# Performance work log

Hardware: AMD Instinct MI355X
Metric: run time of the kernel (lower is better)

## Reference

```python
import jax, jax.numpy as jnp
import numpy as np
import math

B, L, E, H, G = 2, 128, 1024, 16, 8
D = E // H   # head_dim = 64
R = H // G   # query heads per kv head = 2


def setup_inputs() -> dict:
    key = jax.random.key(0)
    ks = jax.random.split(key, 12)
    def nrm(k, shape, s=1.0):
        return jax.random.normal(k, shape, dtype=jnp.float32) * s
    return {
        "Q": nrm(ks[0], (B, L, E)),
        "K": nrm(ks[1], (B, L, E)),
        "V": nrm(ks[2], (B, L, E)),
        "rpe": nrm(ks[3], (B, L, L, E)),
        "ln_g": jnp.ones((E,), jnp.float32),
        "ln_b": jnp.zeros((E,), jnp.float32),
        "Wq": nrm(ks[4], (E, H * D), 0.02), "bq": jnp.zeros((H * D,), jnp.float32),
        "Wk": nrm(ks[5], (E, G * D), 0.02), "bk": jnp.zeros((G * D,), jnp.float32),
        "Wv": nrm(ks[6], (E, G * D), 0.02), "bv": jnp.zeros((G * D,), jnp.float32),
        "Wrk": nrm(ks[7], (E, G * D), 0.02), "brk": jnp.zeros((G * D,), jnp.float32),
        "Wrv": nrm(ks[8], (E, G * D), 0.02), "brv": jnp.zeros((G * D,), jnp.float32),
        "Wo": nrm(ks[9], (E, E), 0.02), "bo": jnp.zeros((E,), jnp.float32),
    }


def _layernorm(x, g, b, eps=1e-5):
    mu = jnp.mean(x, axis=-1, keepdims=True)
    var = jnp.var(x, axis=-1, keepdims=True)
    return (x - mu) * jax.lax.rsqrt(var + eps) * g + b


def reference(Q, K, V, rpe, ln_g, ln_b, Wq, bq, Wk, bk, Wv, bv, Wrk, brk, Wrv, brv, Wo, bo):
    q = (Q @ Wq + bq).reshape(B, L, H, D).transpose(0, 2, 1, 3)   # [B,H,L,D]
    k = (K @ Wk + bk).reshape(B, L, G, D).transpose(0, 2, 1, 3)   # [B,G,L,D]
    v = (V @ Wv + bv).reshape(B, L, G, D).transpose(0, 2, 1, 3)   # [B,G,L,D]

    rn = _layernorm(rpe, ln_g, ln_b)                              # [B,L,L,E]
    rpe_k = (rn @ Wrk + brk).reshape(B, L, L, G, D).transpose(0, 3, 1, 2, 4)  # [B,G,L,L,D]
    rpe_v = (rn @ Wrv + brv).reshape(B, L, L, G, D).transpose(0, 3, 1, 2, 4)

    # Group query heads: head h = g*R + r maps to kv group g (repeat_interleave semantics).
    qg = q.reshape(B, G, R, L, D)
    # score[b,h,i,j] = q[b,h,i] . (k[b,g,i] + rpe_k[b,g,i,j]) / sqrt(D)
    # (note: the original pairs q_i with k_i, only rpe_k carries j-dependence)
    base = jnp.einsum('bgrid,bgid->bgri', qg, k)                  # j-independent q.k
    cross = jnp.einsum('bgrid,bgijd->bgrij', qg, rpe_k)
    scores = (base[..., None] + cross) / math.sqrt(D)             # [B,G,R,L,L]

    # Faithful to F.softmax over flattened L*L axis per head.
    attn = jax.nn.softmax(scores.reshape(B, G, R, L * L), axis=-1).reshape(B, G, R, L, L)

    # qv[b,h,i] = sum_j attn[b,h,i,j] * (v[b,g,i] + rpe_v[b,g,i,j])
    wsum = jnp.sum(attn, axis=-1)                                 # [B,G,R,L]
    qv = wsum[..., None] * v[:, :, None] + jnp.einsum('bgrij,bgijd->bgrid', attn, rpe_v)
    qv = qv.reshape(B, H, L, D).transpose(0, 2, 1, 3).reshape(B, L, E)
    return qv @ Wo + bo
```

## Files before the change

kernel.cpp:

```cpp
#include <hip/hip_runtime.h>


__global__ __launch_bounds__(256) void k_zero(
    const float* __restrict__ bq, const float* __restrict__ bk, const float* __restrict__ bv,
    const float* __restrict__ bo,
    float* __restrict__ q_ws, float* __restrict__ k_ws, float* __restrict__ v_ws,
    float* __restrict__ qv_ws, float* __restrict__ out, float* __restrict__ Gu_ws)
{
  int rr = blockIdx.x, tid = threadIdx.x;
#pragma unroll
  for (int s = 0; s < 4; s++) {
    int i = tid + s * 256;
    q_ws[rr * 1024 + i] = bq[i];
    qv_ws[rr * 1024 + i] = 0.f;
    out[rr * 1024 + i] = bo[i];
  }
#pragma unroll
  for (int s = 0; s < 2; s++) {
    int i = tid + s * 256;
    k_ws[rr * 512 + i] = bk[i];
    v_ws[rr * 512 + i] = bv[i];
  }
  int t = rr * 256 + tid;
  if (t < 4096) Gu_ws[t] = 0.f;
}

__global__ __launch_bounds__(256) void k_qkv(
    const float* __restrict__ Q, const float* __restrict__ K, const float* __restrict__ V,
    const float* __restrict__ Wq, const float* __restrict__ Wk, const float* __restrict__ Wv,
    float* __restrict__ q_ws, float* __restrict__ k_ws, float* __restrict__ v_ws)
{
  __shared__ float xs[32][256];
  int ct = blockIdx.x, rt = blockIdx.y, es = blockIdx.z, tid = threadIdx.x;
  const float* X; const float* W; float* out; int ldW, ldO, c0;
  if (ct < 4)      { X = Q; W = Wq; out = q_ws; ldW = 1024; ldO = 1024; c0 = ct * 256; }
  else if (ct < 6) { X = K; W = Wk; out = k_ws; ldW = 512;  ldO = 512;  c0 = (ct - 4) * 256; }
  else             { X = V; W = Wv; out = v_ws; ldW = 512;  ldO = 512;  c0 = (ct - 6) * 256; }
  int row0 = rt * 32, e0 = es * 256;
  for (int f = tid; f < 2048; f += 256) {
    int r = f >> 6, e4 = f & 63;
    *(float4*)&xs[r][e4 * 4] = *(const float4*)(X + (size_t)(row0 + r) * 1024 + e0 + e4 * 4);
  }
  __syncthreads();
  int cg = tid & 63, rs = tid >> 6;
  int c = c0 + cg * 4;
  float a[8][4];
#pragma unroll
  for (int i = 0; i < 8; i++)
#pragma unroll
    for (int s = 0; s < 4; s++) a[i][s] = 0.f;
  for (int e = 0; e < 256; e++) {
    float4 w4 = *(const float4*)(W + (size_t)(e0 + e) * ldW + c);
#pragma unroll
    for (int i = 0; i < 8; i++) {
      float x = xs[rs * 8 + i][e];
      a[i][0] += x * w4.x; a[i][1] += x * w4.y; a[i][2] += x * w4.z; a[i][3] += x * w4.w;
    }
  }
#pragma unroll
  for (int i = 0; i < 8; i++)
#pragma unroll
    for (int s = 0; s < 4; s++)
      atomicAdd(out + (size_t)(row0 + rs * 8 + i) * ldO + c + s, a[i][s]);
}

__global__ __launch_bounds__(256) void k_base(
    const float* __restrict__ q_ws, const float* __restrict__ k_ws,
    const float* __restrict__ brk, float* __restrict__ S0_ws)
{
  int t = blockIdx.x * 256 + threadIdx.x;
  int r = t >> 4, h = t & 15, g = h >> 1;
  const float* qp = q_ws + r * 1024 + h * 64;
  const float* kp = k_ws + r * 512 + g * 64;
  const float* bp = brk + g * 64;
  float s = 0.f;
  for (int d = 0; d < 64; d++) s += qp[d] * (kp[d] + bp[d]);
  S0_ws[t] = s * 0.125f;
}

__global__ __launch_bounds__(256) void k_uproj(
    const float* __restrict__ q_ws, const float* __restrict__ Wrk,
    const float* __restrict__ lng, const float* __restrict__ lnb,
    float* __restrict__ ut_ws, float* __restrict__ Gu_ws, float* __restrict__ S0_ws)
{
  __shared__ float wt[64][132];
  __shared__ float qs[64][65];
  int et = blockIdx.x, rrt = blockIdx.y, g = blockIdx.z, tid = threadIdx.x;
  int e0 = et * 128, rr0 = rrt * 32;
  for (int f = tid; f < 2048; f += 256) {
    int er = f >> 4, dq = f & 15;
    float4 p = *(const float4*)(Wrk + (size_t)(e0 + er) * 512 + g * 64 + dq * 4);
    wt[dq * 4 + 0][er] = p.x; wt[dq * 4 + 1][er] = p.y;
    wt[dq * 4 + 2][er] = p.z; wt[dq * 4 + 3][er] = p.w;
  }
  for (int f = tid; f < 1024; f += 256) {
    int m = f >> 4, dq = f & 15;
    int rr = rr0 + (m >> 1), h = g * 2 + (m & 1);
    float4 p = *(const float4*)(q_ws + (size_t)rr * 1024 + h * 64 + dq * 4);
    qs[m][dq * 4 + 0] = p.x; qs[m][dq * 4 + 1] = p.y;
    qs[m][dq * 4 + 2] = p.z; qs[m][dq * 4 + 3] = p.w;
  }
  __syncthreads();
  int eg = tid & 31, rs = tid >> 5;
  float acc[8][4];
#pragma unroll
  for (int i = 0; i < 8; i++)
#pragma unroll
    for (int s = 0; s < 4; s++) acc[i][s] = 0.f;
  for (int d = 0; d < 64; d++) {
    float4 wv = *(float4*)&wt[d][eg * 4];
#pragma unroll
    for (int i = 0; i < 8; i++) {
      float qv = qs[rs * 8 + i][d];
      acc[i][0] += qv * wv.x; acc[i][1] += qv * wv.y;
      acc[i][2] += qv * wv.z; acc[i][3] += qv * wv.w;
    }
  }
#pragma unroll
  for (int i = 0; i < 4; i++) {
    int m0 = rs * 8 + 2 * i;
    int rr = rr0 + (m0 >> 1);
#pragma unroll
    for (int s = 0; s < 4; s++) {
      int e = e0 + eg * 4 + s;
      float2 st;
      st.x = acc[2 * i][s] * 0.125f;
      st.y = acc[2 * i + 1][s] * 0.125f;
      *(float2*)(ut_ws + ((size_t)rr * 1024 + e) * 16 + g * 2) = st;
    }
  }
  float4 ge4 = *(const float4*)(lng + e0 + eg * 4);
  float4 be4 = *(const float4*)(lnb + e0 + eg * 4);
#pragma unroll
  for (int i = 0; i < 8; i++) {
    float pg = 0.125f * (ge4.x * acc[i][0] + ge4.y * acc[i][1] + ge4.z * acc[i][2] + ge4.w * acc[i][3]);
    float pb = 0.125f * (be4.x * acc[i][0] + be4.y * acc[i][1] + be4.z * acc[i][2] + be4.w * acc[i][3]);
#pragma unroll
    for (int mk = 16; mk >= 1; mk >>= 1) { pg += __shfl_xor(pg, mk); pb += __shfl_xor(pb, mk); }
    if (eg == 0) {
      int m = rs * 8 + i;
      int rr = rr0 + (m >> 1), h = g * 2 + (m & 1);
      atomicAdd(Gu_ws + rr * 16 + h, pg);
      atomicAdd(S0_ws + rr * 16 + h, pb);
    }
  }
}

__global__ __launch_bounds__(256) void k_dotp(
    const float* __restrict__ rpe, const float* __restrict__ lng,
    const float* __restrict__ ut_ws, const float* __restrict__ Gu_ws,
    const float* __restrict__ S0_ws,
    float* __restrict__ s_ws, float* __restrict__ mu_ws, float* __restrict__ rs_ws)
{
  __shared__ float us[128][16];
  int jt = blockIdx.x, rr = blockIdx.y, tid = threadIdx.x;
  int jl = tid >> 2, hg = tid & 3;
  int j = jt * 64 + jl;
  const float* xrow = rpe + ((size_t)rr * 128 + j) * 1024;
  float acc[4] = {0, 0, 0, 0};
  float sx = 0.f, sq = 0.f;

  for (int ec = 0; ec < 8; ec++) {
    __syncthreads();
    for (int f = tid; f < 512; f += 256) {
      int e = f >> 2, hq = f & 3;
      float4 u4 = *(const float4*)(ut_ws + ((size_t)rr * 1024 + ec * 128 + e) * 16 + hq * 4);
      float ge = lng[ec * 128 + e];
      u4.x *= ge; u4.y *= ge; u4.z *= ge; u4.w *= ge;
      *(float4*)&us[e][hq * 4] = u4;
    }
    __syncthreads();
    const float* xp = xrow + ec * 128;
#pragma unroll 8
    for (int e4 = 0; e4 < 32; e4++) {
      float4 xv = *(const float4*)(xp + e4 * 4);
      float4 u0 = *(float4*)&us[e4 * 4 + 0][hg * 4];
      float4 u1 = *(float4*)&us[e4 * 4 + 1][hg * 4];
      float4 u2 = *(float4*)&us[e4 * 4 + 2][hg * 4];
      float4 u3 = *(float4*)&us[e4 * 4 + 3][hg * 4];
      acc[0] += xv.x * u0.x + xv.y * u1.x + xv.z * u2.x + xv.w * u3.x;
      acc[1] += xv.x * u0.y + xv.y * u1.y + xv.z * u2.y + xv.w * u3.y;
      acc[2] += xv.x * u0.z + xv.y * u1.z + xv.z * u2.z + xv.w * u3.z;
      acc[3] += xv.x * u0.w + xv.y * u1.w + xv.z * u2.w + xv.w * u3.w;
      sx += xv.x + xv.y + xv.z + xv.w;
      sq += xv.x * xv.x + xv.y * xv.y + xv.z * xv.z + xv.w * xv.w;
    }
  }
  float mu = sx * (1.f / 1024.f);
  float rs = rsqrtf(fmaxf(sq * (1.f / 1024.f) - mu * mu, 0.f) + 1e-5f);
  float4 Gu4 = *(const float4*)(Gu_ws + rr * 16 + hg * 4);
  float4 S04 = *(const float4*)(S0_ws + rr * 16 + hg * 4);
  float4 o;
  o.x = S04.x + rs * (acc[0] - mu * Gu4.x);
  o.y = S04.y + rs * (acc[1] - mu * Gu4.y);
  o.z = S04.z + rs * (acc[2] - mu * Gu4.z);
  o.w = S04.w + rs * (acc[3] - mu * Gu4.w);
  *(float4*)(s_ws + ((size_t)rr * 128 + j) * 16 + hg * 4) = o;
  if (hg == 0) { mu_ws[rr * 128 + j] = mu; rs_ws[rr * 128 + j] = rs; }
}

__global__ __launch_bounds__(256) void k_attn_p(
    const float* __restrict__ mu_ws, const float* __restrict__ rs_ws,
    float* __restrict__ s_ws,
    float* __restrict__ M_ws, float* __restrict__ Z_ws, float* __restrict__ C1_ws)
{
  int rr = blockIdx.x, tid = threadIdx.x;
  int h = tid >> 4, jl = tid & 15;
  float sv[8];
  float m = -1e30f;
#pragma unroll
  for (int k = 0; k < 8; k++) {
    int j = jl + k * 16;
    sv[k] = s_ws[((size_t)rr * 128 + j) * 16 + h];
    m = fmaxf(m, sv[k]);
  }
#pragma unroll
  for (int mk = 8; mk >= 1; mk >>= 1) m = fmaxf(m, __shfl_xor(m, mk, 16));
  float z = 0.f, c1 = 0.f;
#pragma unroll
  for (int k = 0; k < 8; k++) {
    int j = jl + k * 16;
    float p = expf(sv[k] - m);
    z += p;
    float p2 = p * rs_ws[rr * 128 + j];
    c1 += p2 * mu_ws[rr * 128 + j];
    s_ws[((size_t)rr * 128 + j) * 16 + h] = p2;
  }
#pragma unroll
  for (int mk = 8; mk >= 1; mk >>= 1) { z += __shfl_xor(z, mk, 16); c1 += __shfl_xor(c1, mk, 16); }
  if (jl == 0) {
    M_ws[rr * 16 + h] = m; Z_ws[rr * 16 + h] = z; C1_ws[rr * 16 + h] = c1;
  }
}

__global__ __launch_bounds__(256) void k_comb(
    const float* __restrict__ M_ws, const float* __restrict__ Z_ws, float* __restrict__ sc_ws)
{
  __shared__ float Mg[32], Zg[32];
  int tid = threadIdx.x;
  if (tid < 32) {
    int b = tid >> 4, h = tid & 15;
    float m = -1e30f;
    for (int i = 0; i < 128; i++) m = fmaxf(m, M_ws[((b << 7) + i) * 16 + h]);
    float z = 0.f;
    for (int i = 0; i < 128; i++) {
      int idx = ((b << 7) + i) * 16 + h;
      z += Z_ws[idx] * expf(M_ws[idx] - m);
    }
    Mg[tid] = m; Zg[tid] = z;
  }
  __syncthreads();
  for (int idx = tid; idx < 4096; idx += 256) {
    int r = idx >> 4, h = idx & 15, b = r >> 7;
    sc_ws[idx] = expf(M_ws[idx] - Mg[b * 16 + h]) / Zg[b * 16 + h];
  }
}

__global__ __launch_bounds__(512) void k_wun(
    const float* __restrict__ rpe, const float* __restrict__ lng, const float* __restrict__ lnb,
    const float* __restrict__ p2_ws,
    const float* __restrict__ Z_ws, const float* __restrict__ C1_ws,
    float* __restrict__ w_ws)
{
  __shared__ float xs[16][516];
  __shared__ float p2s[128][16];
  __shared__ float C1S[16], ZS[16];
  int et = blockIdx.x, rr = blockIdx.y, tid = threadIdx.x;
  int e0 = et * 512;
  if (tid < 512) {
    for (int f = tid; f < 512; f += 512) {
      int j = f >> 2, hq = f & 3;
      *(float4*)&p2s[j][hq * 4] = *(const float4*)(p2_ws + ((size_t)rr * 128 + j) * 16 + hq * 4);
    }
  }
  if (tid < 16) { C1S[tid] = C1_ws[rr * 16 + tid]; ZS[tid] = Z_ws[rr * 16 + tid]; }
  float acc[16];
#pragma unroll
  for (int h = 0; h < 16; h++) acc[h] = 0.f;
  for (int jc = 0; jc < 8; jc++) {
    __syncthreads();
    for (int f = tid; f < 2048; f += 512) {
      int j = f >> 7, e4 = f & 127;
      *(float4*)&xs[j][e4 * 4] =
          *(const float4*)(rpe + ((size_t)(rr * 128 + jc * 16 + j)) * 1024 + e0 + e4 * 4);
    }
    __syncthreads();
#pragma unroll
    for (int j = 0; j < 16; j++) {
      float x = xs[j][tid];
      float4 p0 = *(float4*)&p2s[jc * 16 + j][0];
      float4 p1 = *(float4*)&p2s[jc * 16 + j][4];
      float4 p2 = *(float4*)&p2s[jc * 16 + j][8];
      float4 p3 = *(float4*)&p2s[jc * 16 + j][12];
      acc[0] += x * p0.x; acc[1] += x * p0.y; acc[2] += x * p0.z; acc[3] += x * p0.w;
      acc[4] += x * p1.x; acc[5] += x * p1.y; acc[6] += x * p1.z; acc[7] += x * p1.w;
      acc[8] += x * p2.x; acc[9] += x * p2.y; acc[10] += x * p2.z; acc[11] += x * p2.w;
      acc[12] += x * p3.x; acc[13] += x * p3.y; acc[14] += x * p3.z; acc[15] += x * p3.w;
    }
  }
  int e = e0 + tid;
  float ge = lng[e], be = lnb[e];
  float* wp = w_ws + ((size_t)rr * 1024 + e) * 16;
#pragma unroll
  for (int hq = 0; hq < 4; hq++) {
    float4 o;
    o.x = ge * (acc[hq * 4 + 0] - C1S[hq * 4 + 0]) + be * ZS[hq * 4 + 0];
    o.y = ge * (acc[hq * 4 + 1] - C1S[hq * 4 + 1]) + be * ZS[hq * 4 + 1];
    o.z = ge * (acc[hq * 4 + 2] - C1S[hq * 4 + 2]) + be * ZS[hq * 4 + 2];
    o.w = ge * (acc[hq * 4 + 3] - C1S[hq * 4 + 3]) + be * ZS[hq * 4 + 3];
    *(float4*)(wp + hq * 4) = o;
  }
}

__global__ __launch_bounds__(256) void k_qv(
    const float* __restrict__ w_ws, const float* __restrict__ Wrv,
    float* __restrict__ qv_ws)
{
  __shared__ float As[64][68];
  __shared__ float Ws[64][68];
  int g = blockIdx.x, rrt = blockIdx.y, es = blockIdx.z, tid = threadIdx.x;
  int rr0 = rrt * 32, e0 = es * 256;
  int cl = tid & 15, ms = tid >> 4;
  float acc[4][4];
#pragma unroll
  for (int i = 0; i < 4; i++)
#pragma unroll
    for (int s = 0; s < 4; s++) acc[i][s] = 0.f;
  for (int kc = 0; kc < 4; kc++) {
    __syncthreads();
    for (int f = tid; f < 2048; f += 256) {
      int rl = f >> 6, e = f & 63;
      float2 w2 = *(const float2*)(w_ws + ((size_t)(rr0 + rl) * 1024 + e0 + kc * 64 + e) * 16 + g * 2);
      As[rl * 2 + 0][e] = w2.x;
      As[rl * 2 + 1][e] = w2.y;
    }
    for (int f = tid; f < 1024; f += 256) {
      int e = f >> 4, c4 = f & 15;
      *(float4*)&Ws[e][c4 * 4] =
          *(const float4*)(Wrv + (size_t)(e0 + kc * 64 + e) * 512 + g * 64 + c4 * 4);
    }
    __syncthreads();
    for (int e = 0; e < 64; e++) {
      float4 wv = *(float4*)&Ws[e][cl * 4];
#pragma unroll
      for (int i = 0; i < 4; i++) {
        float a = As[ms * 4 + i][e];
        acc[i][0] += a * wv.x; acc[i][1] += a * wv.y;
        acc[i][2] += a * wv.z; acc[i][3] += a * wv.w;
      }
    }
  }
#pragma unroll
  for (int i = 0; i < 4; i++) {
    int m = ms * 4 + i;
    int rr = rr0 + (m >> 1), hh = m & 1;
    float* qp = qv_ws + (size_t)rr * 1024 + (g * 2 + hh) * 64 + cl * 4;
#pragma unroll
    for (int s = 0; s < 4; s++) atomicAdd(qp + s, acc[i][s]);
  }
}

__global__ __launch_bounds__(256) void k_out(
    const float* __restrict__ qv_ws, const float* __restrict__ v_ws,
    const float* __restrict__ brv, const float* __restrict__ Z_ws,
    const float* __restrict__ sc_ws, const float* __restrict__ Wo,
    float* __restrict__ out)
{
  __shared__ float xs[32][128];
  int ct = blockIdx.x, rt = blockIdx.y, es = blockIdx.z, tid = threadIdx.x;
  int row0 = rt * 32, e0 = es * 128, c0 = ct * 256;
  for (int f = tid; f < 1024; f += 256) {
    int r = f >> 5, e4 = f & 31;
    int row = row0 + r;
#pragma unroll
    for (int s = 0; s < 4; s++) {
      int e = e0 + e4 * 4 + s;
      int h = e >> 6, gg = h >> 1, dl = e & 63;
      float vb = v_ws[row * 512 + gg * 64 + dl] + brv[gg * 64 + dl];
      xs[r][e4 * 4 + s] = sc_ws[row * 16 + h] * (Z_ws[row * 16 + h] * vb + qv_ws[(size_t)row * 1024 + e]);
    }
  }
  __syncthreads();
  int cg = tid & 63, rs = tid >> 6;
  int c = c0 + cg * 4;
  float a[8][4];
#pragma unroll
  for (int i = 0; i < 8; i++)
#pragma unroll
    for (int s = 0; s < 4; s++) a[i][s] = 0.f;
  for (int e = 0; e < 128; e++) {
    float4 w4 = *(const float4*)(Wo + (size_t)(e0 + e) * 1024 + c);
#pragma unroll
    for (int i = 0; i < 8; i++) {
      float x = xs[rs * 8 + i][e];
      a[i][0] += x * w4.x; a[i][1] += x * w4.y; a[i][2] += x * w4.z; a[i][3] += x * w4.w;
    }
  }
#pragma unroll
  for (int i = 0; i < 8; i++)
#pragma unroll
    for (int s = 0; s < 4; s++)
      atomicAdd(out + (size_t)(row0 + rs * 8 + i) * 1024 + c + s, a[i][s]);
}

extern "C" void kernel_launch(void* const* d_in, const int* in_sizes, int n_in,
                              void* d_out, int out_size, void* d_ws, size_t ws_size,
                              hipStream_t stream) {
  (void)in_sizes; (void)n_in; (void)out_size; (void)ws_size;
  const float* Q   = (const float*)d_in[0];
  const float* K   = (const float*)d_in[1];
  const float* V   = (const float*)d_in[2];
  const float* rpe = (const float*)d_in[3];
  const float* lng = (const float*)d_in[4];
  const float* lnb = (const float*)d_in[5];
  const float* Wq  = (const float*)d_in[6];
  const float* bq  = (const float*)d_in[7];
  const float* Wk  = (const float*)d_in[8];
  const float* bk  = (const float*)d_in[9];
  const float* Wv  = (const float*)d_in[10];
  const float* bv  = (const float*)d_in[11];
  const float* Wrk = (const float*)d_in[12];
  const float* brk = (const float*)d_in[13];
  const float* Wrv = (const float*)d_in[14];
  const float* brv = (const float*)d_in[15];
  const float* Wo  = (const float*)d_in[16];
  const float* bo  = (const float*)d_in[17];
  float* out = (float*)d_out;

  float* ws    = (float*)d_ws;
  float* q_ws  = ws;
  float* k_ws  = q_ws + 262144;
  float* v_ws  = k_ws + 131072;
  float* ut_ws = v_ws + 131072;
  float* S0_ws = ut_ws + 4194304;
  float* Gu_ws = S0_ws + 4096;
  float* s_ws  = Gu_ws + 4096;
  float* mu_ws = s_ws + 524288;
  float* rs_ws = mu_ws + 32768;
  float* M_ws  = rs_ws + 32768;
  float* Z_ws  = M_ws + 4096;
  float* C1_ws = Z_ws + 4096;
  float* sc_ws = C1_ws + 4096;
  float* qv_ws = sc_ws + 4096;
  float* w_ws  = ut_ws;

  k_zero<<<256, 256, 0, stream>>>(bq, bk, bv, bo, q_ws, k_ws, v_ws, qv_ws, out, Gu_ws);
  k_qkv<<<dim3(8, 8, 4), 256, 0, stream>>>(Q, K, V, Wq, Wk, Wv, q_ws, k_ws, v_ws);
  k_base<<<16, 256, 0, stream>>>(q_ws, k_ws, brk, S0_ws);
  k_uproj<<<dim3(8, 8, 8), 256, 0, stream>>>(q_ws, Wrk, lng, lnb, ut_ws, Gu_ws, S0_ws);
  k_dotp<<<dim3(2, 256), 256, 0, stream>>>(rpe, lng, ut_ws, Gu_ws, S0_ws, s_ws, mu_ws, rs_ws);
  k_attn_p<<<256, 256, 0, stream>>>(mu_ws, rs_ws, s_ws, M_ws, Z_ws, C1_ws);
  k_comb<<<1, 256, 0, stream>>>(M_ws, Z_ws, sc_ws);
  k_wun<<<dim3(2, 256), 512, 0, stream>>>(rpe, lng, lnb, s_ws, Z_ws, C1_ws, w_ws);
  k_qv<<<dim3(8, 8, 4), 256, 0, stream>>>(w_ws, Wrv, qv_ws);
  k_out<<<dim3(4, 8, 8), 256, 0, stream>>>(qv_ws, v_ws, brv, Z_ws, sc_ws, Wo, out);
}
```

Measured before the change: 575.3 us.

## Shrink per-block tiles across GEMM kernels and parallelize softmax combine

Most kernels are retiled to use smaller per-block row tiles with more blocks: qkv, uproj, dotp, wun, qv and out. The GEMM-style kernels now software-prefetch the next weight row into registers. k_comb moves from a single block to 32 blocks with tree reductions, k_base loads with float4, and k_qv drops its shared-memory weight tile in favour of direct prefetched global loads. The goal is more parallelism and occupancy on a wide GPU, at the cost of more redundant weight reads and more atomics.

```diff
diff --git a/kernel.cpp b/kernel.cpp
--- a/kernel.cpp
+++ b/kernel.cpp
@@ -30,38 +30,36 @@
     const float* __restrict__ Wq, const float* __restrict__ Wk, const float* __restrict__ Wv,
     float* __restrict__ q_ws, float* __restrict__ k_ws, float* __restrict__ v_ws)
 {
-  __shared__ float xs[32][256];
+  __shared__ float xs[8][256];
   int ct = blockIdx.x, rt = blockIdx.y, es = blockIdx.z, tid = threadIdx.x;
   const float* X; const float* W; float* out; int ldW, ldO, c0;
   if (ct < 4)      { X = Q; W = Wq; out = q_ws; ldW = 1024; ldO = 1024; c0 = ct * 256; }
   else if (ct < 6) { X = K; W = Wk; out = k_ws; ldW = 512;  ldO = 512;  c0 = (ct - 4) * 256; }
   else             { X = V; W = Wv; out = v_ws; ldW = 512;  ldO = 512;  c0 = (ct - 6) * 256; }
-  int row0 = rt * 32, e0 = es * 256;
-  for (int f = tid; f < 2048; f += 256) {
+  int row0 = rt * 8, e0 = es * 256;
+  for (int f = tid; f < 512; f += 256) {
     int r = f >> 6, e4 = f & 63;
     *(float4*)&xs[r][e4 * 4] = *(const float4*)(X + (size_t)(row0 + r) * 1024 + e0 + e4 * 4);
   }
   __syncthreads();
   int cg = tid & 63, rs = tid >> 6;
   int c = c0 + cg * 4;
-  float a[8][4];
-#pragma unroll
-  for (int i = 0; i < 8; i++)
-#pragma unroll
-    for (int s = 0; s < 4; s++) a[i][s] = 0.f;
+  const float* wp = W + (size_t)e0 * ldW + c;
+  float a0[4] = {0, 0, 0, 0}, a1[4] = {0, 0, 0, 0};
+  float4 wc = *(const float4*)wp;
   for (int e = 0; e < 256; e++) {
-    float4 w4 = *(const float4*)(W + (size_t)(e0 + e) * ldW + c);
-#pragma unroll
-    for (int i = 0; i < 8; i++) {
-      float x = xs[rs * 8 + i][e];
-      a[i][0] += x * w4.x; a[i][1] += x * w4.y; a[i][2] += x * w4.z; a[i][3] += x * w4.w;
-    }
-  }
-#pragma unroll
-  for (int i = 0; i < 8; i++)
-#pragma unroll
-    for (int s = 0; s < 4; s++)
-      atomicAdd(out + (size_t)(row0 + rs * 8 + i) * ldO + c + s, a[i][s]);
+    int en = e + 1 < 256 ? e + 1 : 255;
+    float4 wn = *(const float4*)(wp + (size_t)en * ldW);
+    float x0 = xs[rs][e], x1 = xs[rs + 4][e];
+    a0[0] += x0 * wc.x; a0[1] += x0 * wc.y; a0[2] += x0 * wc.z; a0[3] += x0 * wc.w;
+    a1[0] += x1 * wc.x; a1[1] += x1 * wc.y; a1[2] += x1 * wc.z; a1[3] += x1 * wc.w;
+    wc = wn;
+  }
+#pragma unroll
+  for (int s = 0; s < 4; s++) {
+    atomicAdd(out + (size_t)(row0 + rs) * ldO + c + s, a0[s]);
+    atomicAdd(out + (size_t)(row0 + rs + 4) * ldO + c + s, a1[s]);
+  }
 }
 
 __global__ __launch_bounds__(256) void k_base(
@@ -74,7 +72,14 @@
   const float* kp = k_ws + r * 512 + g * 64;
   const float* bp = brk + g * 64;
   float s = 0.f;
-  for (int d = 0; d < 64; d++) s += qp[d] * (kp[d] + bp[d]);
+#pragma unroll
+  for (int d4 = 0; d4 < 16; d4++) {
+    float4 q4 = *(const float4*)(qp + d4 * 4);
+    float4 k4 = *(const float4*)(kp + d4 * 4);
+    float4 b4 = *(const float4*)(bp + d4 * 4);
+    s += q4.x * (k4.x + b4.x) + q4.y * (k4.y + b4.y)
+       + q4.z * (k4.z + b4.z) + q4.w * (k4.w + b4.w);
+  }
   S0_ws[t] = s * 0.125f;
 }
 
@@ -83,17 +88,17 @@
     const float* __restrict__ lng, const float* __restrict__ lnb,
     float* __restrict__ ut_ws, float* __restrict__ Gu_ws, float* __restrict__ S0_ws)
 {
-  __shared__ float wt[64][132];
-  __shared__ float qs[64][65];
+  __shared__ float wt[64][128];
+  __shared__ float qs[32][64];
   int et = blockIdx.x, rrt = blockIdx.y, g = blockIdx.z, tid = threadIdx.x;
-  int e0 = et * 128, rr0 = rrt * 32;
+  int e0 = et * 128, rr0 = rrt * 16;
   for (int f = tid; f < 2048; f += 256) {
     int er = f >> 4, dq = f & 15;
     float4 p = *(const float4*)(Wrk + (size_t)(e0 + er) * 512 + g * 64 + dq * 4);
     wt[dq * 4 + 0][er] = p.x; wt[dq * 4 + 1][er] = p.y;
     wt[dq * 4 + 2][er] = p.z; wt[dq * 4 + 3][er] = p.w;
   }
-  for (int f = tid; f < 1024; f += 256) {
+  for (int f = tid; f < 512; f += 256) {
     int m = f >> 4, dq = f & 15;
     int rr = rr0 + (m >> 1), h = g * 2 + (m & 1);
     float4 p = *(const float4*)(q_ws + (size_t)rr * 1024 + h * 64 + dq * 4);
@@ -102,43 +107,42 @@
   }
   __syncthreads();
   int eg = tid & 31, rs = tid >> 5;
-  float acc[8][4];
-#pragma unroll
-  for (int i = 0; i < 8; i++)
+  float acc[4][4];
+#pragma unroll
+  for (int i = 0; i < 4; i++)
 #pragma unroll
     for (int s = 0; s < 4; s++) acc[i][s] = 0.f;
   for (int d = 0; d < 64; d++) {
     float4 wv = *(float4*)&wt[d][eg * 4];
 #pragma unroll
-    for (int i = 0; i < 8; i++) {
-      float qv = qs[rs * 8 + i][d];
+    for (int i = 0; i < 4; i++) {
+      float qv = qs[rs * 4 + i][d];
       acc[i][0] += qv * wv.x; acc[i][1] += qv * wv.y;
       acc[i][2] += qv * wv.z; acc[i][3] += qv * wv.w;
     }
   }
 #pragma unroll
-  for (int i = 0; i < 4; i++) {
-    int m0 = rs * 8 + 2 * i;
-    int rr = rr0 + (m0 >> 1);
+  for (int k = 0; k < 2; k++) {
+    int rr = rr0 + rs * 2 + k;
 #pragma unroll
     for (int s = 0; s < 4; s++) {
       int e = e0 + eg * 4 + s;
       float2 st;
-      st.x = acc[2 * i][s] * 0.125f;
-      st.y = acc[2 * i + 1][s] * 0.125f;
+      st.x = acc[2 * k][s] * 0.125f;
+      st.y = acc[2 * k + 1][s] * 0.125f;
       *(float2*)(ut_ws + ((size_t)rr * 1024 + e) * 16 + g * 2) = st;
     }
   }
   float4 ge4 = *(const float4*)(lng + e0 + eg * 4);
   float4 be4 = *(const float4*)(lnb + e0 + eg * 4);
 #pragma unroll
-  for (int i = 0; i < 8; i++) {
+  for (int i = 0; i < 4; i++) {
     float pg = 0.125f * (ge4.x * acc[i][0] + ge4.y * acc[i][1] + ge4.z * acc[i][2] + ge4.w * acc[i][3]);
     float pb = 0.125f * (be4.x * acc[i][0] + be4.y * acc[i][1] + be4.z * acc[i][2] + be4.w * acc[i][3]);
 #pragma unroll
     for (int mk = 16; mk >= 1; mk >>= 1) { pg += __shfl_xor(pg, mk); pb += __shfl_xor(pb, mk); }
     if (eg == 0) {
-      int m = rs * 8 + i;
+      int m = rs * 4 + i;
       int rr = rr0 + (m >> 1), h = g * 2 + (m & 1);
       atomicAdd(Gu_ws + rr * 16 + h, pg);
       atomicAdd(S0_ws + rr * 16 + h, pb);
@@ -146,33 +150,33 @@
   }
 }
 
-__global__ __launch_bounds__(256) void k_dotp(
+__global__ __launch_bounds__(128) void k_dotp(
     const float* __restrict__ rpe, const float* __restrict__ lng,
     const float* __restrict__ ut_ws, const float* __restrict__ Gu_ws,
     const float* __restrict__ S0_ws,
     float* __restrict__ s_ws, float* __restrict__ mu_ws, float* __restrict__ rs_ws)
 {
-  __shared__ float us[128][16];
+  __shared__ float us[256][16];
   int jt = blockIdx.x, rr = blockIdx.y, tid = threadIdx.x;
   int jl = tid >> 2, hg = tid & 3;
-  int j = jt * 64 + jl;
+  int j = jt * 32 + jl;
   const float* xrow = rpe + ((size_t)rr * 128 + j) * 1024;
   float acc[4] = {0, 0, 0, 0};
   float sx = 0.f, sq = 0.f;
 
-  for (int ec = 0; ec < 8; ec++) {
-    __syncthreads();
-    for (int f = tid; f < 512; f += 256) {
+  for (int ec = 0; ec < 4; ec++) {
+    __syncthreads();
+    for (int f = tid; f < 1024; f += 128) {
       int e = f >> 2, hq = f & 3;
-      float4 u4 = *(const float4*)(ut_ws + ((size_t)rr * 1024 + ec * 128 + e) * 16 + hq * 4);
-      float ge = lng[ec * 128 + e];
+      float4 u4 = *(const float4*)(ut_ws + ((size_t)rr * 1024 + ec * 256 + e) * 16 + hq * 4);
+      float ge = lng[ec * 256 + e];
       u4.x *= ge; u4.y *= ge; u4.z *= ge; u4.w *= ge;
       *(float4*)&us[e][hq * 4] = u4;
     }
     __syncthreads();
-    const float* xp = xrow + ec * 128;
-#pragma unroll 8
-    for (int e4 = 0; e4 < 32; e4++) {
+    const float* xp = xrow + ec * 256;
+#pragma unroll 4
+    for (int e4 = 0; e4 < 64; e4++) {
       float4 xv = *(const float4*)(xp + e4 * 4);
       float4 u0 = *(float4*)&us[e4 * 4 + 0][hg * 4];
       float4 u1 = *(float4*)&us[e4 * 4 + 1][hg * 4];
@@ -233,45 +237,47 @@
   }
 }
 
-__global__ __launch_bounds__(256) void k_comb(
+__global__ __launch_bounds__(128) void k_comb(
     const float* __restrict__ M_ws, const float* __restrict__ Z_ws, float* __restrict__ sc_ws)
 {
-  __shared__ float Mg[32], Zg[32];
-  int tid = threadIdx.x;
-  if (tid < 32) {
-    int b = tid >> 4, h = tid & 15;
-    float m = -1e30f;
-    for (int i = 0; i < 128; i++) m = fmaxf(m, M_ws[((b << 7) + i) * 16 + h]);
-    float z = 0.f;
-    for (int i = 0; i < 128; i++) {
-      int idx = ((b << 7) + i) * 16 + h;
-      z += Z_ws[idx] * expf(M_ws[idx] - m);
-    }
-    Mg[tid] = m; Zg[tid] = z;
-  }
-  __syncthreads();
-  for (int idx = tid; idx < 4096; idx += 256) {
-    int r = idx >> 4, h = idx & 15, b = r >> 7;
-    sc_ws[idx] = expf(M_ws[idx] - Mg[b * 16 + h]) / Zg[b * 16 + h];
-  }
-}
-
-__global__ __launch_bounds__(512) void k_wun(
+  __shared__ float red[128];
+  int b = blockIdx.x >> 4, h = blockIdx.x & 15;
+  int i = threadIdx.x;
+  int idx = ((b << 7) + i) * 16 + h;
+  float ml = M_ws[idx];
+  red[i] = ml;
+  __syncthreads();
+  for (int s = 64; s >= 1; s >>= 1) {
+    if (i < s) red[i] = fmaxf(red[i], red[i + s]);
+    __syncthreads();
+  }
+  float mg = red[0];
+  __syncthreads();
+  float zl = Z_ws[idx] * expf(ml - mg);
+  red[i] = zl;
+  __syncthreads();
+  for (int s = 64; s >= 1; s >>= 1) {
+    if (i < s) red[i] += red[i + s];
+    __syncthreads();
+  }
+  float zg = red[0];
+  sc_ws[idx] = expf(ml - mg) / zg;
+}
+
+__global__ __launch_bounds__(256) void k_wun(
     const float* __restrict__ rpe, const float* __restrict__ lng, const float* __restrict__ lnb,
     const float* __restrict__ p2_ws,
     const float* __restrict__ Z_ws, const float* __restrict__ C1_ws,
     float* __restrict__ w_ws)
 {
-  __shared__ float xs[16][516];
+  __shared__ float xs[16][256];
   __shared__ float p2s[128][16];
   __shared__ float C1S[16], ZS[16];
   int et = blockIdx.x, rr = blockIdx.y, tid = threadIdx.x;
-  int e0 = et * 512;
-  if (tid < 512) {
-    for (int f = tid; f < 512; f += 512) {
-      int j = f >> 2, hq = f & 3;
-      *(float4*)&p2s[j][hq * 4] = *(const float4*)(p2_ws + ((size_t)rr * 128 + j) * 16 + hq * 4);
-    }
+  int e0 = et * 256;
+  for (int f = tid; f < 512; f += 256) {
+    int j = f >> 2, hq = f & 3;
+    *(float4*)&p2s[j][hq * 4] = *(const float4*)(p2_ws + ((size_t)rr * 128 + j) * 16 + hq * 4);
   }
   if (tid < 16) { C1S[tid] = C1_ws[rr * 16 + tid]; ZS[tid] = Z_ws[rr * 16 + tid]; }
   float acc[16];
@@ -279,8 +285,8 @@
   for (int h = 0; h < 16; h++) acc[h] = 0.f;
   for (int jc = 0; jc < 8; jc++) {
     __syncthreads();
-    for (int f = tid; f < 2048; f += 512) {
-      int j = f >> 7, e4 = f & 127;
+    for (int f = tid; f < 1024; f += 256) {
+      int j = f >> 6, e4 = f & 63;
       *(float4*)&xs[j][e4 * 4] =
           *(const float4*)(rpe + ((size_t)(rr * 128 + jc * 16 + j)) * 1024 + e0 + e4 * 4);
     }
@@ -316,47 +322,38 @@
     const float* __restrict__ w_ws, const float* __restrict__ Wrv,
     float* __restrict__ qv_ws)
 {
-  __shared__ float As[64][68];
-  __shared__ float Ws[64][68];
+  __shared__ float As[32][133];
   int g = blockIdx.x, rrt = blockIdx.y, es = blockIdx.z, tid = threadIdx.x;
-  int rr0 = rrt * 32, e0 = es * 256;
+  int rr0 = rrt * 16, e0 = es * 128;
+  for (int f = tid; f < 2048; f += 256) {
+    int rl = f >> 7, e = f & 127;
+    float2 w2 = *(const float2*)(w_ws + ((size_t)(rr0 + rl) * 1024 + e0 + e) * 16 + g * 2);
+    As[rl * 2 + 0][e] = w2.x;
+    As[rl * 2 + 1][e] = w2.y;
+  }
+  __syncthreads();
   int cl = tid & 15, ms = tid >> 4;
-  float acc[4][4];
-#pragma unroll
-  for (int i = 0; i < 4; i++)
-#pragma unroll
-    for (int s = 0; s < 4; s++) acc[i][s] = 0.f;
-  for (int kc = 0; kc < 4; kc++) {
-    __syncthreads();
-    for (int f = tid; f < 2048; f += 256) {
-      int rl = f >> 6, e = f & 63;
-      float2 w2 = *(const float2*)(w_ws + ((size_t)(rr0 + rl) * 1024 + e0 + kc * 64 + e) * 16 + g * 2);
-      As[rl * 2 + 0][e] = w2.x;
-      As[rl * 2 + 1][e] = w2.y;
-    }
-    for (int f = tid; f < 1024; f += 256) {
-      int e = f >> 4, c4 = f & 15;
-      *(float4*)&Ws[e][c4 * 4] =
-          *(const float4*)(Wrv + (size_t)(e0 + kc * 64 + e) * 512 + g * 64 + c4 * 4);
-    }
-    __syncthreads();
-    for (int e = 0; e < 64; e++) {
-      float4 wv = *(float4*)&Ws[e][cl * 4];
-#pragma unroll
-      for (int i = 0; i < 4; i++) {
-        float a = As[ms * 4 + i][e];
-        acc[i][0] += a * wv.x; acc[i][1] += a * wv.y;
-        acc[i][2] += a * wv.z; acc[i][3] += a * wv.w;
-      }
-    }
-  }
-#pragma unroll
-  for (int i = 0; i < 4; i++) {
-    int m = ms * 4 + i;
-    int rr = rr0 + (m >> 1), hh = m & 1;
+  const float* wp = Wrv + (size_t)e0 * 512 + g * 64 + cl * 4;
+  float acc[2][4];
+#pragma unroll
+  for (int hh = 0; hh < 2; hh++)
+#pragma unroll
+    for (int s = 0; s < 4; s++) acc[hh][s] = 0.f;
+  float4 wc = *(const float4*)wp;
+  for (int e = 0; e < 128; e++) {
+    int en = e + 1 < 128 ? e + 1 : 127;
+    float4 wn = *(const float4*)(wp + (size_t)en * 512);
+    float a0 = As[ms * 2][e], a1 = As[ms * 2 + 1][e];
+    acc[0][0] += a0 * wc.x; acc[0][1] += a0 * wc.y; acc[0][2] += a0 * wc.z; acc[0][3] += a0 * wc.w;
+    acc[1][0] += a1 * wc.x; acc[1][1] += a1 * wc.y; acc[1][2] += a1 * wc.z; acc[1][3] += a1 * wc.w;
+    wc = wn;
+  }
+  int rr = rr0 + ms;
+#pragma unroll
+  for (int hh = 0; hh < 2; hh++) {
     float* qp = qv_ws + (size_t)rr * 1024 + (g * 2 + hh) * 64 + cl * 4;
 #pragma unroll
-    for (int s = 0; s < 4; s++) atomicAdd(qp + s, acc[i][s]);
+    for (int s = 0; s < 4; s++) atomicAdd(qp + s, acc[hh][s]);
   }
 }
 
@@ -366,41 +363,35 @@
     const float* __restrict__ sc_ws, const float* __restrict__ Wo,
     float* __restrict__ out)
 {
-  __shared__ float xs[32][128];
+  __shared__ float xs[8][128];
   int ct = blockIdx.x, rt = blockIdx.y, es = blockIdx.z, tid = threadIdx.x;
-  int row0 = rt * 32, e0 = es * 128, c0 = ct * 256;
+  int row0 = rt * 8, e0 = es * 128, c0 = ct * 256;
   for (int f = tid; f < 1024; f += 256) {
-    int r = f >> 5, e4 = f & 31;
-    int row = row0 + r;
-#pragma unroll
-    for (int s = 0; s < 4; s++) {
-      int e = e0 + e4 * 4 + s;
-      int h = e >> 6, gg = h >> 1, dl = e & 63;
-      float vb = v_ws[row * 512 + gg * 64 + dl] + brv[gg * 64 + dl];
-      xs[r][e4 * 4 + s] = sc_ws[row * 16 + h] * (Z_ws[row * 16 + h] * vb + qv_ws[(size_t)row * 1024 + e]);
-    }
+    int r = f >> 7, ei = f & 127;
+    int e = e0 + ei, row = row0 + r;
+    int h = e >> 6, gg = h >> 1, dl = e & 63;
+    float vb = v_ws[row * 512 + gg * 64 + dl] + brv[gg * 64 + dl];
+    xs[r][ei] = sc_ws[row * 16 + h] * (Z_ws[row * 16 + h] * vb + qv_ws[(size_t)row * 1024 + e]);
   }
   __syncthreads();
   int cg = tid & 63, rs = tid >> 6;
   int c = c0 + cg * 4;
-  float a[8][4];
-#pragma unroll
-  for (int i = 0; i < 8; i++)
-#pragma unroll
-    for (int s = 0; s < 4; s++) a[i][s] = 0.f;
+  const float* wp = Wo + (size_t)e0 * 1024 + c;
+  float a0[4] = {0, 0, 0, 0}, a1[4] = {0, 0, 0, 0};
+  float4 wc = *(const float4*)wp;
   for (int e = 0; e < 128; e++) {
-    float4 w4 = *(const float4*)(Wo + (size_t)(e0 + e) * 1024 + c);
-#pragma unroll
-    for (int i = 0; i < 8; i++) {
-      float x = xs[rs * 8 + i][e];
-      a[i][0] += x * w4.x; a[i][1] += x * w4.y; a[i][2] += x * w4.z; a[i][3] += x * w4.w;
-    }
-  }
-#pragma unroll
-  for (int i = 0; i < 8; i++)
-#pragma unroll
-    for (int s = 0; s < 4; s++)
-      atomicAdd(out + (size_t)(row0 + rs * 8 + i) * 1024 + c + s, a[i][s]);
+    int en = e + 1 < 128 ? e + 1 : 127;
+    float4 wn = *(const float4*)(wp + (size_t)en * 1024);
+    float x0 = xs[rs][e], x1 = xs[rs + 4][e];
+    a0[0] += x0 * wc.x; a0[1] += x0 * wc.y; a0[2] += x0 * wc.z; a0[3] += x0 * wc.w;
+    a1[0] += x1 * wc.x; a1[1] += x1 * wc.y; a1[2] += x1 * wc.z; a1[3] += x1 * wc.w;
+    wc = wn;
+  }
+#pragma unroll
+  for (int s = 0; s < 4; s++) {
+    atomicAdd(out + (size_t)(row0 + rs) * 1024 + c + s, a0[s]);
+    atomicAdd(out + (size_t)(row0 + rs + 4) * 1024 + c + s, a1[s]);
+  }
 }
 
 extern "C" void kernel_launch(void* const* d_in, const int* in_sizes, int n_in,
@@ -445,13 +436,13 @@
   float* w_ws  = ut_ws;
 
   k_zero<<<256, 256, 0, stream>>>(bq, bk, bv, bo, q_ws, k_ws, v_ws, qv_ws, out, Gu_ws);
-  k_qkv<<<dim3(8, 8, 4), 256, 0, stream>>>(Q, K, V, Wq, Wk, Wv, q_ws, k_ws, v_ws);
+  k_qkv<<<dim3(8, 32, 4), 256, 0, stream>>>(Q, K, V, Wq, Wk, Wv, q_ws, k_ws, v_ws);
   k_base<<<16, 256, 0, stream>>>(q_ws, k_ws, brk, S0_ws);
-  k_uproj<<<dim3(8, 8, 8), 256, 0, stream>>>(q_ws, Wrk, lng, lnb, ut_ws, Gu_ws, S0_ws);
-  k_dotp<<<dim3(2, 256), 256, 0, stream>>>(rpe, lng, ut_ws, Gu_ws, S0_ws, s_ws, mu_ws, rs_ws);
+  k_uproj<<<dim3(8, 16, 8), 256, 0, stream>>>(q_ws, Wrk, lng, lnb, ut_ws, Gu_ws, S0_ws);
+  k_dotp<<<dim3(4, 256), 128, 0, stream>>>(rpe, lng, ut_ws, Gu_ws, S0_ws, s_ws, mu_ws, rs_ws);
   k_attn_p<<<256, 256, 0, stream>>>(mu_ws, rs_ws, s_ws, M_ws, Z_ws, C1_ws);
-  k_comb<<<1, 256, 0, stream>>>(M_ws, Z_ws, sc_ws);
-  k_wun<<<dim3(2, 256), 512, 0, stream>>>(rpe, lng, lnb, s_ws, Z_ws, C1_ws, w_ws);
-  k_qv<<<dim3(8, 8, 4), 256, 0, stream>>>(w_ws, Wrv, qv_ws);
-  k_out<<<dim3(4, 8, 8), 256, 0, stream>>>(qv_ws, v_ws, brv, Z_ws, sc_ws, Wo, out);
-}
+  k_comb<<<32, 128, 0, stream>>>(M_ws, Z_ws, sc_ws);
+  k_wun<<<dim3(4, 256), 256, 0, stream>>>(rpe, lng, lnb, s_ws, Z_ws, C1_ws, w_ws);
+  k_qv<<<dim3(8, 16, 8), 256, 0, stream>>>(w_ws, Wrv, qv_ws);
+  k_out<<<dim3(4, 32, 8), 256, 0, stream>>>(qv_ws, v_ws, brv, Z_ws, sc_ws, Wo, out);
+}
```

Result: faster. 508.3 us (-11.6%).
